# Optimization experiments

Measured on AMD Instinct MI355X. Metric: run time of the kernel, lower is better.

The kernel has to match this reference:

```python
import jax, jax.numpy as jnp
import numpy as np

N_NODES = 100_000
N_EDGES = 3_200_000
IN_FEATS = 256
HIDDEN = 256
N_CLASSES = 64
K_HOPS = 3


def setup_inputs() -> dict:
    key = jax.random.key(0)
    ks = jax.random.split(key, 6)
    features = jax.random.normal(ks[0], (N_NODES, IN_FEATS), dtype=jnp.float32)
    edge_src = jax.random.randint(ks[1], (N_EDGES,), 0, N_NODES, dtype=jnp.int32)
    edge_dst = jax.random.randint(ks[2], (N_EDGES,), 0, N_NODES, dtype=jnp.int32)
    ln_gamma = jnp.ones((IN_FEATS,), jnp.float32)
    ln_beta = jnp.zeros((IN_FEATS,), jnp.float32)
    # Kaiming-ish small init so repeated propagation stays numerically tame
    W_conv = jax.random.normal(ks[3], (HIDDEN, IN_FEATS), jnp.float32) * (1.0 / np.sqrt(IN_FEATS))
    b_conv = jnp.zeros((HIDDEN,), jnp.float32)
    W_fc = jax.random.normal(ks[4], (N_CLASSES, HIDDEN), jnp.float32) * (1.0 / np.sqrt(HIDDEN))
    b_fc = jnp.zeros((N_CLASSES,), jnp.float32)
    return {
        "features": features, "edge_src": edge_src, "edge_dst": edge_dst,
        "ln_gamma": ln_gamma, "ln_beta": ln_beta,
        "W_conv": W_conv, "b_conv": b_conv, "W_fc": W_fc, "b_fc": b_fc,
    }


def _layer_norm(x, gamma, beta, eps=1e-5):
    mu = jnp.mean(x, axis=-1, keepdims=True)
    var = jnp.var(x, axis=-1, keepdims=True)
    return (x - mu) * jax.lax.rsqrt(var + eps) * gamma + beta


def reference(features, edge_src, edge_dst, ln_gamma, ln_beta, W_conv, b_conv, W_fc, b_fc):
    n = features.shape[0]
    # LayerNorm over feature dim
    h = _layer_norm(features, ln_gamma, ln_beta)
    # symmetric normalization D^{-1/2} A D^{-1/2} (DGL SGConv norm='both',
    # using in-degrees, clamped to >= 1)
    deg = jax.ops.segment_sum(jnp.ones_like(edge_dst, dtype=h.dtype), edge_dst, num_segments=n)
    norm = jax.lax.rsqrt(jnp.clip(deg, 1.0, None))[:, None]  # [N, 1]
    # k-hop propagation: h <- norm * (A @ (norm * h))
    for _ in range(K_HOPS):
        h = norm * jax.ops.segment_sum((h * norm)[edge_src], edge_dst, num_segments=n)
    # SGConv linear, then ReLU (dropout is identity in eval), then classifier fc
    h = h @ W_conv.T + b_conv
    h = jax.nn.relu(h)
    return h @ W_fc.T + b_fc
```

## Files before the change

kernel.cpp:

```cpp
#include <hip/hip_runtime.h>
#include <hip/hip_bf16.h>

#define NND 100000
#define NED 3200000
#define F 256
#define NCLS 64
#define NC 98
#define MAXPER 36864
#define EBLK 4096

typedef _Float16 f16x8 __attribute__((ext_vector_type(8)));
typedef _Float16 f16x4 __attribute__((ext_vector_type(4)));
typedef float f32x4 __attribute__((ext_vector_type(4)));

__global__ void k_init(int* __restrict__ gcur) {
    int b = threadIdx.x;
    if (b < NC) gcur[b] = b * MAXPER;
}

__global__ __launch_bounds__(256) void k_passA(const int* __restrict__ src, const int* __restrict__ dst,
                                               int* __restrict__ gcur, int2* __restrict__ binned) {
    __shared__ int hist[NC], scn[NC], cur[NC], gbase[NC];
    __shared__ int2 stage[EBLK];
    __shared__ unsigned char bkt[EBLK];
    int base = blockIdx.x * EBLK;
    int n = NED - base; if (n > EBLK) n = EBLK;
    int t = threadIdx.x;
    if (t < NC) hist[t] = 0;
    __syncthreads();
    for (int i = t; i < n; i += 256) atomicAdd(&hist[dst[base + i] >> 10], 1);
    __syncthreads();
    if (t == 0) {
        int run = 0;
        for (int b = 0; b < NC; b++) { scn[b] = run; cur[b] = run; run += hist[b]; }
    }
    __syncthreads();
    if (t < NC) gbase[t] = atomicAdd(&gcur[t], hist[t]);
    __syncthreads();
    for (int i = t; i < n; i += 256) {
        int s = src[base + i], d = dst[base + i];
        int b = d >> 10;
        int r = atomicAdd(&cur[b], 1);
        stage[r] = make_int2(s, d);
        bkt[r] = (unsigned char)b;
    }
    __syncthreads();
    for (int i = t; i < n; i += 256) {
        int b = bkt[i];
        binned[gbase[b] + (i - scn[b])] = stage[i];
    }
}

__global__ void k_cscan(const int* __restrict__ gcur, int* __restrict__ cbase) {
    if (threadIdx.x == 0) {
        int run = 0;
        for (int b = 0; b < NC; b++) { cbase[b] = run; run += gcur[b] - b * MAXPER; }
        cbase[NC] = run;
    }
}

__global__ __launch_bounds__(1024) void k_passB(const int2* __restrict__ binned, const int* __restrict__ cbase,
                                                int* __restrict__ deg, int* __restrict__ start,
                                                float* __restrict__ norm, int* __restrict__ col) {
    __shared__ int h[1024], sh[1024], cur[1024];
    int b = blockIdx.x;
    int t = threadIdx.x;
    int n0 = b << 10;
    const int2* eb = binned + (size_t)b * MAXPER;
    int c0 = cbase[b];
    int cnt = cbase[b + 1] - c0;
    h[t] = 0;
    __syncthreads();
    for (int i = t; i < cnt; i += 1024) atomicAdd(&h[eb[i].y - n0], 1);
    __syncthreads();
    sh[t] = h[t];
    __syncthreads();
    for (int off = 1; off < 1024; off <<= 1) {
        int v = (t >= off) ? sh[t - off] : 0;
        __syncthreads();
        sh[t] += v;
        __syncthreads();
    }
    int lofs = sh[t] - h[t];
    cur[t] = lofs;
    int node = n0 + t;
    if (node < NND) {
        int d = h[t];
        deg[node] = d;
        start[node] = c0 + lofs;
        float df = (float)d;
        norm[node] = rsqrtf(df < 1.0f ? 1.0f : df);
    }
    __syncthreads();
    for (int i = t; i < cnt; i += 1024) {
        int2 e = eb[i];
        int r = atomicAdd(&cur[e.y - n0], 1);
        col[c0 + r] = e.x;
    }
}

__global__ __launch_bounds__(256) void k_ln(const float* __restrict__ x, const float* __restrict__ gamma,
                                            const float* __restrict__ beta, const float* __restrict__ norm,
                                            _Float16* __restrict__ y) {
    int node = blockIdx.x * 4 + (threadIdx.x >> 6);
    int lane = threadIdx.x & 63;
    if (node >= NND) return;
    float4 v = ((const float4*)x)[node * 64 + lane];
    float s = v.x + v.y + v.z + v.w;
    float s2 = v.x * v.x + v.y * v.y + v.z * v.z + v.w * v.w;
    for (int m = 1; m < 64; m <<= 1) {
        s += __shfl_xor(s, m, 64);
        s2 += __shfl_xor(s2, m, 64);
    }
    float mu = s * (1.0f / 256.0f);
    float var = s2 * (1.0f / 256.0f) - mu * mu;
    float rs = rsqrtf(var + 1e-5f);
    float w = norm[node];
    float4 g = ((const float4*)gamma)[lane];
    float4 b = ((const float4*)beta)[lane];
    f16x4 o;
    o[0] = (_Float16)(w * ((v.x - mu) * rs * g.x + b.x));
    o[1] = (_Float16)(w * ((v.y - mu) * rs * g.y + b.y));
    o[2] = (_Float16)(w * ((v.z - mu) * rs * g.z + b.z));
    o[3] = (_Float16)(w * ((v.w - mu) * rs * g.w + b.w));
    *(f16x4*)(y + (size_t)node * F + lane * 4) = o;
}

template <int LAST>
__global__ __launch_bounds__(256) void k_hop(const _Float16* __restrict__ x, _Float16* __restrict__ y,
                                             const int* __restrict__ start, const int* __restrict__ deg,
                                             const int* __restrict__ col, const float* __restrict__ norm) {
    int node = __builtin_amdgcn_readfirstlane(blockIdx.x * 4 + (threadIdx.x >> 6));
    if (node >= NND) return;
    int lane = threadIdx.x & 63;
    int hf = lane >> 5;
    int l = lane & 31;
    int s0 = start[node];
    int cnt = deg[node];
    float acc[8] = {0.f, 0.f, 0.f, 0.f, 0.f, 0.f, 0.f, 0.f};
    for (int base = 0; base < cnt; base += 64) {
        int rem = cnt - base;
        int cv = (lane < rem) ? col[s0 + base + lane] : 0;
        int npair = rem > 64 ? 32 : (rem >> 1);
#pragma unroll 2
        for (int i = 0; i < npair; i++) {
            int s = __shfl(cv, 2 * i + hf, 64);
            f16x8 v = *(const f16x8*)(x + (size_t)s * F + l * 8);
#pragma unroll
            for (int j = 0; j < 8; j++) acc[j] += (float)v[j];
        }
        if ((rem & 1) && rem <= 64) {
            int s = __shfl(cv, rem - 1, 64);
            if (hf == 0) {
                f16x8 v = *(const f16x8*)(x + (size_t)s * F + l * 8);
#pragma unroll
                for (int j = 0; j < 8; j++) acc[j] += (float)v[j];
            }
        }
    }
#pragma unroll
    for (int j = 0; j < 8; j++) acc[j] += __shfl_xor(acc[j], 32, 64);
    if (hf == 0) {
        float wd = norm[node];
        float sc = LAST ? wd : wd * wd;
        f16x8 o;
#pragma unroll
        for (int j = 0; j < 8; j++) o[j] = (_Float16)(acc[j] * sc);
        *(f16x8*)(y + (size_t)node * F + (size_t)l * 8) = o;
    }
}

__global__ __launch_bounds__(256) void k_castW(const float4* __restrict__ Wc, const float4* __restrict__ Wf,
                                               f16x4* __restrict__ WcO, f16x4* __restrict__ WfO) {
    int i = blockIdx.x * 256 + threadIdx.x;
    if (i < F * F / 4) {
        float4 v = Wc[i];
        f16x4 o;
        o[0] = (_Float16)v.x; o[1] = (_Float16)v.y; o[2] = (_Float16)v.z; o[3] = (_Float16)v.w;
        WcO[i] = o;
    } else {
        int j = i - F * F / 4;
        if (j < NCLS * F / 4) {
            float4 v = Wf[j];
            f16x4 o;
            o[0] = (_Float16)v.x; o[1] = (_Float16)v.y; o[2] = (_Float16)v.z; o[3] = (_Float16)v.w;
            WfO[j] = o;
        }
    }
}

__global__ __launch_bounds__(256) void k_gemm(const _Float16* __restrict__ A,
                                              const _Float16* __restrict__ Wc, const float* __restrict__ bc,
                                              const _Float16* __restrict__ Wf, const float* __restrict__ bf,
                                              float* __restrict__ out) {
    __shared__ _Float16 mid[16][264];
    int wave = threadIdx.x >> 6, lane = threadIdx.x & 63;
    int l15 = lane & 15, lhi = lane >> 4;
    int row0 = blockIdx.x * 16;
    const _Float16* arow = A + (size_t)(row0 + l15) * F + lhi * 8;
    int ncol0 = wave * 64;
    f32x4 acc[4];
    for (int t = 0; t < 4; t++) acc[t] = (f32x4){0.f, 0.f, 0.f, 0.f};
#pragma unroll
    for (int kt = 0; kt < 8; kt++) {
        f16x8 a = *(const f16x8*)(arow + kt * 32);
#pragma unroll
        for (int t = 0; t < 4; t++) {
            int n = ncol0 + t * 16 + l15;
            f16x8 b = *(const f16x8*)(Wc + (size_t)n * F + lhi * 8 + kt * 32);
            acc[t] = __builtin_amdgcn_mfma_f32_16x16x32_f16(a, b, acc[t], 0, 0, 0);
        }
    }
#pragma unroll
    for (int t = 0; t < 4; t++) {
        int colb = ncol0 + t * 16 + l15;
        float bv = bc[colb];
#pragma unroll
        for (int r = 0; r < 4; r++) {
            float v = acc[t][r] + bv;
            mid[lhi * 4 + r][colb] = (_Float16)(v > 0.f ? v : 0.f);
        }
    }
    __syncthreads();
    f32x4 acc2 = (f32x4){0.f, 0.f, 0.f, 0.f};
    int colb = wave * 16 + l15;
    const _Float16* brow = Wf + (size_t)colb * F + lhi * 8;
#pragma unroll
    for (int kt = 0; kt < 8; kt++) {
        f16x8 a = *(const f16x8*)&mid[l15][lhi * 8 + kt * 32];
        f16x8 b = *(const f16x8*)(brow + kt * 32);
        acc2 = __builtin_amdgcn_mfma_f32_16x16x32_f16(a, b, acc2, 0, 0, 0);
    }
    float bv = bf[colb];
#pragma unroll
    for (int r = 0; r < 4; r++) {
        int row = row0 + lhi * 4 + r;
        out[(size_t)row * NCLS + colb] = acc2[r] + bv;
    }
}

extern "C" void kernel_launch(void* const* d_in, const int* in_sizes, int n_in,
                              void* d_out, int out_size, void* d_ws, size_t ws_size,
                              hipStream_t stream) {
    const float* features = (const float*)d_in[0];
    const int* edge_src = (const int*)d_in[1];
    const int* edge_dst = (const int*)d_in[2];
    const float* ln_gamma = (const float*)d_in[3];
    const float* ln_beta = (const float*)d_in[4];
    const float* W_conv = (const float*)d_in[5];
    const float* b_conv = (const float*)d_in[6];
    const float* W_fc = (const float*)d_in[7];
    const float* b_fc = (const float*)d_in[8];
    float* out = (float*)d_out;

    char* w = (char*)d_ws;
    const size_t HB2 = (size_t)NND * F * 2;
    _Float16* hA = (_Float16*)(w + 0);
    int2* binned = (int2*)(w + 0);
    _Float16* hB = (_Float16*)(w + HB2);
    int* col = (int*)(w + 102400000);
    int* deg = (int*)(w + 115200000);
    int* start = (int*)(w + 115600000);
    float* norm = (float*)(w + 116000000);
    int* gcur = (int*)(w + 116400000);
    int* cbase = (int*)(w + 116401024);
    _Float16* Wc16 = (_Float16*)(w + 116402176);
    _Float16* Wf16 = (_Float16*)(w + 116533248);

    k_init<<<1, 128, 0, stream>>>(gcur);
    k_passA<<<(NED + EBLK - 1) / EBLK, 256, 0, stream>>>(edge_src, edge_dst, gcur, binned);
    k_cscan<<<1, 64, 0, stream>>>(gcur, cbase);
    k_passB<<<NC, 1024, 0, stream>>>(binned, cbase, deg, start, norm, col);

    k_ln<<<NND / 4, 256, 0, stream>>>(features, ln_gamma, ln_beta, norm, hA);

    k_hop<0><<<NND / 4, 256, 0, stream>>>(hA, hB, start, deg, col, norm);
    k_hop<0><<<NND / 4, 256, 0, stream>>>(hB, hA, start, deg, col, norm);
    k_hop<1><<<NND / 4, 256, 0, stream>>>(hA, hB, start, deg, col, norm);

    k_castW<<<(F * F / 4 + NCLS * F / 4 + 255) / 256, 256, 0, stream>>>(
        (const float4*)W_conv, (const float4*)W_fc, (f16x4*)Wc16, (f16x4*)Wf16);

    k_gemm<<<NND / 16, 256, 0, stream>>>(hB, Wc16, b_conv, Wf16, b_fc, out);
}
```

Measured before the change: 892.5 us.

## Restructure SpMM hops into source-banded LDS accumulation with cross-block phase barrier

Edges are now binned into 1000-node destination chunks and sub-sorted by 25-node destination group and 16K-node source band. Each hop is split into two feature halves, and each block accumulates 400 destination nodes in fp16 LDS. A soft grid-wide barrier keeps all blocks on the same source band, aiming for L2 locality of gathered rows. The cost is fp16 accumulation (precision risk), a spin barrier that gives up after a bounded wait, and six launches instead of three.

```diff
diff --git a/kernel.cpp b/kernel.cpp
--- a/kernel.cpp
+++ b/kernel.cpp
@@ -5,12 +5,15 @@
 #define NED 3200000
 #define F 256
 #define NCLS 64
-#define NC 98
-#define MAXPER 36864
+#define NC 100
+#define MAXPER 36000
 #define EBLK 4096
+#define NSB 7
+#define HOPBLK 250
 
 typedef _Float16 f16x8 __attribute__((ext_vector_type(8)));
 typedef _Float16 f16x4 __attribute__((ext_vector_type(4)));
+typedef _Float16 f16x2 __attribute__((ext_vector_type(2)));
 typedef float f32x4 __attribute__((ext_vector_type(4)));
 
 __global__ void k_init(int* __restrict__ gcur) {
@@ -28,7 +31,7 @@
     int t = threadIdx.x;
     if (t < NC) hist[t] = 0;
     __syncthreads();
-    for (int i = t; i < n; i += 256) atomicAdd(&hist[dst[base + i] >> 10], 1);
+    for (int i = t; i < n; i += 256) atomicAdd(&hist[dst[base + i] / 1000], 1);
     __syncthreads();
     if (t == 0) {
         int run = 0;
@@ -39,7 +42,7 @@
     __syncthreads();
     for (int i = t; i < n; i += 256) {
         int s = src[base + i], d = dst[base + i];
-        int b = d >> 10;
+        int b = d / 1000;
         int r = atomicAdd(&cur[b], 1);
         stage[r] = make_int2(s, d);
         bkt[r] = (unsigned char)b;
@@ -51,51 +54,69 @@
     }
 }
 
-__global__ void k_cscan(const int* __restrict__ gcur, int* __restrict__ cbase) {
-    if (threadIdx.x == 0) {
-        int run = 0;
-        for (int b = 0; b < NC; b++) { cbase[b] = run; run += gcur[b] - b * MAXPER; }
-        cbase[NC] = run;
-    }
-}
-
-__global__ __launch_bounds__(1024) void k_passB(const int2* __restrict__ binned, const int* __restrict__ cbase,
-                                                int* __restrict__ deg, int* __restrict__ start,
-                                                float* __restrict__ norm, int* __restrict__ col) {
-    __shared__ int h[1024], sh[1024], cur[1024];
+__global__ __launch_bounds__(1024) void k_passB(const int2* __restrict__ binned, const int* __restrict__ gcur,
+                                                float* __restrict__ norm, int* __restrict__ col2,
+                                                int* __restrict__ ebs, int* __restrict__ ebc) {
+    __shared__ int h[7000], cur[7000], psum[1024];
     int b = blockIdx.x;
     int t = threadIdx.x;
-    int n0 = b << 10;
+    int n = gcur[b] - b * MAXPER;
     const int2* eb = binned + (size_t)b * MAXPER;
-    int c0 = cbase[b];
-    int cnt = cbase[b + 1] - c0;
-    h[t] = 0;
-    __syncthreads();
-    for (int i = t; i < cnt; i += 1024) atomicAdd(&h[eb[i].y - n0], 1);
-    __syncthreads();
-    sh[t] = h[t];
+    for (int k = t; k < 7000; k += 1024) h[k] = 0;
+    __syncthreads();
+    for (int i = t; i < n; i += 1024) {
+        int2 e = eb[i];
+        int dl = e.y - b * 1000;
+        int lw = dl / 25, ln = dl - lw * 25;
+        int sb = e.x >> 14;
+        atomicAdd(&h[lw * 175 + sb * 25 + ln], 1);
+    }
+    __syncthreads();
+    if (t < 1000) {
+        int lw = t / 25, ln = t - lw * 25;
+        int d = 0;
+#pragma unroll
+        for (int sb = 0; sb < NSB; sb++) d += h[lw * 175 + sb * 25 + ln];
+        float df = (float)d;
+        norm[b * 1000 + t] = rsqrtf(df < 1.0f ? 1.0f : df);
+    }
+    __syncthreads();
+    int c[7] = {0, 0, 0, 0, 0, 0, 0};
+    int s = 0;
+    if (t < 1000) {
+#pragma unroll
+        for (int k = 0; k < 7; k++) { c[k] = h[t * 7 + k]; s += c[k]; }
+    }
+    psum[t] = s;
     __syncthreads();
     for (int off = 1; off < 1024; off <<= 1) {
-        int v = (t >= off) ? sh[t - off] : 0;
+        int v = (t >= off) ? psum[t - off] : 0;
         __syncthreads();
-        sh[t] += v;
+        psum[t] += v;
         __syncthreads();
     }
-    int lofs = sh[t] - h[t];
-    cur[t] = lofs;
-    int node = n0 + t;
-    if (node < NND) {
-        int d = h[t];
-        deg[node] = d;
-        start[node] = c0 + lofs;
-        float df = (float)d;
-        norm[node] = rsqrtf(df < 1.0f ? 1.0f : df);
-    }
-    __syncthreads();
-    for (int i = t; i < cnt; i += 1024) {
+    if (t < 1000) {
+        int run = psum[t] - s;
+#pragma unroll
+        for (int k = 0; k < 7; k++) { h[t * 7 + k] = run; cur[t * 7 + k] = run; run += c[k]; }
+    }
+    __syncthreads();
+    if (t < 280) {
+        int lw = t / 7, sb = t - lw * 7;
+        int k0 = lw * 175 + sb * 25;
+        int st = h[k0];
+        int en = (k0 + 25 < 7000) ? h[k0 + 25] : n;
+        ebs[(40 * b + lw) * NSB + sb] = b * MAXPER + st;
+        ebc[(40 * b + lw) * NSB + sb] = en - st;
+    }
+    __syncthreads();
+    for (int i = t; i < n; i += 1024) {
         int2 e = eb[i];
-        int r = atomicAdd(&cur[e.y - n0], 1);
-        col[c0 + r] = e.x;
+        int dl = e.y - b * 1000;
+        int lw = dl / 25, ln = dl - lw * 25;
+        int sb = e.x >> 14;
+        int r = atomicAdd(&cur[lw * 175 + sb * 25 + ln], 1);
+        col2[b * MAXPER + r] = (e.x << 5) | ln;
     }
 }
 
@@ -127,46 +148,56 @@
 }
 
 template <int LAST>
-__global__ __launch_bounds__(256) void k_hop(const _Float16* __restrict__ x, _Float16* __restrict__ y,
-                                             const int* __restrict__ start, const int* __restrict__ deg,
-                                             const int* __restrict__ col, const float* __restrict__ norm) {
-    int node = __builtin_amdgcn_readfirstlane(blockIdx.x * 4 + (threadIdx.x >> 6));
-    if (node >= NND) return;
-    int lane = threadIdx.x & 63;
-    int hf = lane >> 5;
-    int l = lane & 31;
-    int s0 = start[node];
-    int cnt = deg[node];
-    float acc[8] = {0.f, 0.f, 0.f, 0.f, 0.f, 0.f, 0.f, 0.f};
-    for (int base = 0; base < cnt; base += 64) {
-        int rem = cnt - base;
-        int cv = (lane < rem) ? col[s0 + base + lane] : 0;
-        int npair = rem > 64 ? 32 : (rem >> 1);
-#pragma unroll 2
-        for (int i = 0; i < npair; i++) {
-            int s = __shfl(cv, 2 * i + hf, 64);
-            f16x8 v = *(const f16x8*)(x + (size_t)s * F + l * 8);
-#pragma unroll
-            for (int j = 0; j < 8; j++) acc[j] += (float)v[j];
-        }
-        if ((rem & 1) && rem <= 64) {
-            int s = __shfl(cv, rem - 1, 64);
-            if (hf == 0) {
-                f16x8 v = *(const f16x8*)(x + (size_t)s * F + l * 8);
-#pragma unroll
-                for (int j = 0; j < 8; j++) acc[j] += (float)v[j];
+__global__ __launch_bounds__(1024) void k_hop2(const _Float16* __restrict__ x, _Float16* __restrict__ y,
+                                               const int* __restrict__ ebs, const int* __restrict__ ebc,
+                                               const int* __restrict__ col2, const float* __restrict__ norm,
+                                               int P, int* __restrict__ bar) {
+    __shared__ _Float16 accu[400 * 128];
+    int t = threadIdx.x;
+    int wave = t >> 6, lane = t & 63;
+    int gw = blockIdx.x * 16 + wave;
+    for (int i = t; i < 25600; i += 1024) ((int*)accu)[i] = 0;
+    __syncthreads();
+    const _Float16* xb = x + P * 128;
+    for (int sb = 0; sb < NSB; sb++) {
+        int e0 = ebs[gw * NSB + sb];
+        int e1 = e0 + ebc[gw * NSB + sb];
+        for (int base = e0; base < e1; base += 64) {
+            int m = e1 - base; if (m > 64) m = 64;
+            int cv = col2[base + (lane < m ? lane : m - 1)];
+            for (int j = 0; j < m; j++) {
+                int wrd = __shfl(cv, j, 64);
+                int ln = wrd & 31;
+                int srcn = wrd >> 5;
+                f16x2 v = *(const f16x2*)(xb + (size_t)srcn * F + lane * 2);
+                f16x2* p = (f16x2*)&accu[((wave * 25 + ln) << 7) + lane * 2];
+                *p = *p + v;
             }
         }
-    }
-#pragma unroll
-    for (int j = 0; j < 8; j++) acc[j] += __shfl_xor(acc[j], 32, 64);
-    if (hf == 0) {
+        if (sb < NSB - 1) {
+            __syncthreads();
+            if (t == 0) {
+                __hip_atomic_fetch_add(bar, 1, __ATOMIC_RELAXED, __HIP_MEMORY_SCOPE_AGENT);
+                int target = HOPBLK * (sb + 1);
+                int it = 0;
+                while (__hip_atomic_load(bar, __ATOMIC_RELAXED, __HIP_MEMORY_SCOPE_AGENT) < target
+                       && ++it < 4096)
+                    __builtin_amdgcn_s_sleep(4);
+            }
+            __syncthreads();
+        }
+    }
+    __syncthreads();
+    for (int i = t; i < 400 * 64; i += 1024) {
+        int nl = i >> 6, lp = i & 63;
+        int node = blockIdx.x * 400 + nl;
         float wd = norm[node];
         float sc = LAST ? wd : wd * wd;
-        f16x8 o;
-#pragma unroll
-        for (int j = 0; j < 8; j++) o[j] = (_Float16)(acc[j] * sc);
-        *(f16x8*)(y + (size_t)node * F + (size_t)l * 8) = o;
+        f16x2 a = *(f16x2*)&accu[(nl << 7) + lp * 2];
+        f16x2 o;
+        o[0] = (_Float16)((float)a[0] * sc);
+        o[1] = (_Float16)((float)a[1] * sc);
+        *(f16x2*)(y + (size_t)node * F + P * 128 + lp * 2) = o;
     }
 }
 
@@ -258,25 +289,28 @@
     _Float16* hA = (_Float16*)(w + 0);
     int2* binned = (int2*)(w + 0);
     _Float16* hB = (_Float16*)(w + HB2);
-    int* col = (int*)(w + 102400000);
-    int* deg = (int*)(w + 115200000);
-    int* start = (int*)(w + 115600000);
-    float* norm = (float*)(w + 116000000);
-    int* gcur = (int*)(w + 116400000);
-    int* cbase = (int*)(w + 116401024);
-    _Float16* Wc16 = (_Float16*)(w + 116402176);
-    _Float16* Wf16 = (_Float16*)(w + 116533248);
+    int* col2 = (int*)(w + 102400000);
+    float* norm = (float*)(w + 117000000);
+    int* ebs = (int*)(w + 117400000);
+    int* ebc = (int*)(w + 117520000);
+    int* gcur = (int*)(w + 117640000);
+    int* bar = (int*)(w + 117642048);
+    _Float16* Wc16 = (_Float16*)(w + 117643072);
+    _Float16* Wf16 = (_Float16*)(w + 117774144);
 
     k_init<<<1, 128, 0, stream>>>(gcur);
     k_passA<<<(NED + EBLK - 1) / EBLK, 256, 0, stream>>>(edge_src, edge_dst, gcur, binned);
-    k_cscan<<<1, 64, 0, stream>>>(gcur, cbase);
-    k_passB<<<NC, 1024, 0, stream>>>(binned, cbase, deg, start, norm, col);
+    k_passB<<<NC, 1024, 0, stream>>>(binned, gcur, norm, col2, ebs, ebc);
 
     k_ln<<<NND / 4, 256, 0, stream>>>(features, ln_gamma, ln_beta, norm, hA);
 
-    k_hop<0><<<NND / 4, 256, 0, stream>>>(hA, hB, start, deg, col, norm);
-    k_hop<0><<<NND / 4, 256, 0, stream>>>(hB, hA, start, deg, col, norm);
-    k_hop<1><<<NND / 4, 256, 0, stream>>>(hA, hB, start, deg, col, norm);
+    hipMemsetAsync(bar, 0, 64, stream);
+    k_hop2<0><<<HOPBLK, 1024, 0, stream>>>(hA, hB, ebs, ebc, col2, norm, 0, bar + 0);
+    k_hop2<0><<<HOPBLK, 1024, 0, stream>>>(hA, hB, ebs, ebc, col2, norm, 1, bar + 1);
+    k_hop2<0><<<HOPBLK, 1024, 0, stream>>>(hB, hA, ebs, ebc, col2, norm, 0, bar + 2);
+    k_hop2<0><<<HOPBLK, 1024, 0, stream>>>(hB, hA, ebs, ebc, col2, norm, 1, bar + 3);
+    k_hop2<1><<<HOPBLK, 1024, 0, stream>>>(hA, hB, ebs, ebc, col2, norm, 0, bar + 4);
+    k_hop2<1><<<HOPBLK, 1024, 0, stream>>>(hA, hB, ebs, ebc, col2, norm, 1, bar + 5);
 
     k_castW<<<(F * F / 4 + NCLS * F / 4 + 255) / 256, 256, 0, stream>>>(
         (const float4*)W_conv, (const float4*)W_fc, (f16x4*)Wc16, (f16x4*)Wf16);
```

After: 2.214 ms. 148% more time.
